# Performance work log

Hardware: AMD Instinct MI355X
Metric: run time of the kernel (lower is better)

## Reference

```python
import jax, jax.numpy as jnp
import numpy as np

RES = 100          # resolution
ITERS = 1000       # lowfid solver iterations
INIT_MIN = 0.01    # conductivity floor (init_min)
BATCH = 32
HIDDEN = [128, 256, 512]


def conductivity_original(pores, res):
    """Coarse 5x5 pore map -> base conductivity on the fine res x res grid.
    pore present (1) -> low conductivity (0), solid (0) -> conductivity 1."""
    B = pores.shape[0]
    grid = 1.0 - pores.reshape(B, 5, 5)
    f = res // 5
    return jnp.repeat(jnp.repeat(grid, f, axis=1), f, axis=2)  # (B, res, res)


def mlp_forward(x, params):
    n = len(params)
    for i, (W, b) in enumerate(params):
        x = x @ W + b
        if i < n - 1:
            x = jax.nn.relu(x)
    return x


def lowfid_solve(k):
    """1000-iteration Jacobi relaxation of variable-coefficient steady heat
    equation with T=1 on top edge, T=0 on bottom edge, insulated sides.
    Returns effective conductivity kappa per sample, shape (B,)."""
    B, res, _ = k.shape
    # face conductivities (arithmetic mean of adjacent cells, edge-padded)
    kp = jnp.pad(k, ((0, 0), (1, 1), (1, 1)), mode='edge')
    kN = 0.5 * (k + kp[:, :-2, 1:-1])
    kS = 0.5 * (k + kp[:, 2:, 1:-1])
    kW = 0.5 * (k + kp[:, 1:-1, :-2])
    kE = 0.5 * (k + kp[:, 1:-1, 2:])
    denom = kN + kS + kW + kE + 1e-12

    def step(T, _):
        Tp = jnp.pad(T, ((0, 0), (0, 0), (1, 1)), mode='edge')        # side Neumann
        Tp = jnp.pad(Tp, ((0, 0), (1, 1), (0, 0)))                    # top/bottom Dirichlet
        Tp = Tp.at[:, 0, :].set(1.0)                                   # T=1 at top, T=0 at bottom
        T_new = (kN * Tp[:, :-2, 1:-1] + kS * Tp[:, 2:, 1:-1]
                 + kW * Tp[:, 1:-1, :-2] + kE * Tp[:, 1:-1, 2:]) / denom
        return T_new, None

    T0 = jnp.broadcast_to(jnp.linspace(1.0, 0.0, res)[None, :, None], (B, res, res))
    T, _ = jax.lax.scan(step, T0, None, length=ITERS)
    # heat flux through top boundary; domain size 1, dT = 1 -> kappa = mean flux
    kappa = jnp.mean(2.0 * res * k[:, 0, :] * (1.0 - T[:, 0, :]), axis=1)
    return kappa


def setup_inputs() -> dict:
    key = jax.random.key(0)
    ks = jax.random.split(key, 10)
    pores = (jax.random.uniform(ks[0], (BATCH, 25)) > 0.5).astype(jnp.float32)
    sizes = [25] + HIDDEN + [RES * RES]
    inp = {"pores": pores}
    for i in range(len(sizes) - 1):
        fan_in = sizes[i]
        W = jax.random.normal(ks[1 + 2 * i], (sizes[i], sizes[i + 1]), jnp.float32) * np.sqrt(2.0 / fan_in)
        b = jnp.zeros((sizes[i + 1],), jnp.float32)
        inp[f"W{i + 1}"] = W
        inp[f"b{i + 1}"] = b
    return inp


def reference(pores, W1, b1, W2, b2, W3, b3, W4, b4):
    params = [(W1, b1), (W2, b2), (W3, b3), (W4, b4)]
    B = pores.shape[0]
    gen = mlp_forward(pores.reshape(B, 25), params).reshape(B, RES, RES)
    cond = gen + conductivity_original(pores, RES)   # learn_residual
    cond = jnp.maximum(cond, INIT_MIN)               # relu clamp to init_min
    kappa = lowfid_solve(cond)
    return kappa, cond
```

## Files before the change

kernel.cpp:

```cpp
#include <hip/hip_runtime.h>
#include <hip/hip_bf16.h>

#define RES   100
#define ITERS 1000
#define SLOTP 128

typedef float vf2 __attribute__((ext_vector_type(2)));

__global__ __launch_bounds__(256) void mlp123(const float* __restrict__ pores,
                                              const float* __restrict__ W1, const float* __restrict__ b1,
                                              const float* __restrict__ W2, const float* __restrict__ b2,
                                              const float* __restrict__ W3, const float* __restrict__ b3,
                                              float* __restrict__ x3out) {
    __shared__ float x1[128];
    __shared__ float x2[256];
    const int s = blockIdx.x, tid = threadIdx.x;

    if (tid < 128) {
        float acc = b1[tid];
#pragma unroll
        for (int k = 0; k < 25; ++k)
            acc = fmaf(pores[s * 25 + k], W1[k * 128 + tid], acc);
        x1[tid] = fmaxf(acc, 0.0f);
    }
    __syncthreads();

    {
        float acc = b2[tid];
#pragma unroll 8
        for (int k = 0; k < 128; ++k)
            acc = fmaf(x1[k], W2[k * 256 + tid], acc);
        x2[tid] = fmaxf(acc, 0.0f);
    }
    __syncthreads();

    {
        float a0 = b3[tid], a1 = b3[tid + 256];
#pragma unroll 8
        for (int k = 0; k < 256; ++k) {
            float xv = x2[k];
            a0 = fmaf(xv, W3[k * 512 + tid],       a0);
            a1 = fmaf(xv, W3[k * 512 + tid + 256], a1);
        }
        x3out[s * 512 + tid]       = fmaxf(a0, 0.0f);
        x3out[s * 512 + tid + 256] = fmaxf(a1, 0.0f);
    }
}

__global__ __launch_bounds__(256) void fc4_fused(const float* __restrict__ X3,
                                                 const float* __restrict__ W4,
                                                 const float* __restrict__ b4,
                                                 const float* __restrict__ pores,
                                                 float* __restrict__ cond) {
    const int j = blockIdx.x * 256 + threadIdx.x;
    if (j >= RES * RES) return;
    const int bg = blockIdx.y;
    const float* x = X3 + bg * 8 * 512;

    float acc[8];
    float bj = b4[j];
#pragma unroll
    for (int b = 0; b < 8; ++b) acc[b] = bj;

    for (int k0 = 0; k0 < 512; k0 += 8) {
        float w[8];
#pragma unroll
        for (int u = 0; u < 8; ++u)
            w[u] = W4[(k0 + u) * (RES * RES) + j];
#pragma unroll
        for (int u = 0; u < 8; ++u) {
#pragma unroll
            for (int b = 0; b < 8; ++b)
                acc[b] = fmaf(x[b * 512 + k0 + u], w[u], acc[b]);
        }
    }

    const int row = j / RES, col = j % RES;
    const int p = (row / 20) * 5 + (col / 20);
#pragma unroll
    for (int b = 0; b < 8; ++b) {
        int bb = bg * 8 + b;
        float base = 1.0f - pores[bb * 25 + p];
        cond[bb * RES * RES + j] = fmaxf(acc[b] + base, 0.01f);
    }
}

__device__ __forceinline__ float dpp_shr1_z(float src) {
    return __int_as_float(__builtin_amdgcn_update_dpp(
        0, __float_as_int(src), 0x138, 0xf, 0xf, true));
}
__device__ __forceinline__ float dpp_shl1_z(float src) {
    return __int_as_float(__builtin_amdgcn_update_dpp(
        0, __float_as_int(src), 0x130, 0xf, 0xf, true));
}

__device__ __forceinline__ vf2 jrowT(vf2 wv, vf2 ev, vf2 c,
                                     vf2 wWr, vf2 wEr, vf2 wPr, vf2 wTr, vf2 Cr) {
    float nlo = dpp_shr1_z(c.y);
    float shi = dpp_shl1_z(c.x);
    vf2 P;  P.x  = nlo; P.y  = shi;
    vf2 TS; TS.x = c.y; TS.y = c.x;
    return Cr + wPr * P + wTr * TS + wWr * wv + wEr * ev;
}

template<int R>
__device__ __forceinline__ void jstepT(const vf2* __restrict__ wptr, const vf2* __restrict__ eptr,
                                       vf2* __restrict__ topptr, vf2* __restrict__ botptr,
                                       const vf2* wW, const vf2* wE,
                                       const vf2* wP, const vf2* wT, const vf2* C,
                                       const vf2* Tin, vf2* Tout) {
    vf2 wval = *wptr;
    vf2 eval = *eptr;
#pragma unroll
    for (int r = 0; r < R; ++r) {
        vf2 wv = (r == 0)     ? wval : Tin[r - 1];
        vf2 ev = (r == R - 1) ? eval : Tin[r + 1];
        Tout[r] = jrowT(wv, ev, Tin[r], wW[r], wE[r], wP[r], wT[r], C[r]);
        if (r == 0) *topptr = Tout[0];
    }
    *botptr = Tout[R - 1];
}

__global__ __launch_bounds__(1024) void jacobi(const float* __restrict__ cond,
                                               float* __restrict__ kappa_out) {
    __shared__ float kst[RES * RES];
    __shared__ float SA[32 * SLOTP];
    __shared__ float SB[32 * SLOTP];
    __shared__ float red[16];

    const int b   = blockIdx.x;
    const int tid = threadIdx.x;

    for (int i = tid; i < RES * RES; i += 1024)
        kst[i] = cond[b * RES * RES + i];
    __syncthreads();

    const int w    = tid >> 6;
    const int lane = tid & 63;
    const int R    = (w < 4) ? 7 : 6;
    const int c0   = (w < 4) ? 7 * w : 28 + 6 * (w - 4);
    const int l    = min(lane, 49);
    const int i0   = 2 * l, i1 = 2 * l + 1;
    const int lane2 = 2 * lane;

    vf2 wW[7], wE[7], wP[7], wT[7], C[7], T0[7], T1[7];

#pragma unroll
    for (int r = 0; r < 7; ++r) {
        if (r < R) {
            int c  = c0 + r;
            int in_ = i0 ? i0 - 1 : 0;
            int is_ = (i1 < RES - 1) ? i1 + 1 : RES - 1;
            int jw  = c ? c - 1 : 0;
            int je  = (c < RES - 1) ? c + 1 : RES - 1;
            float kc0 = kst[i0 * RES + c], kc1 = kst[i1 * RES + c];
            float kn0 = 0.5f * (kc0 + kst[in_ * RES + c]);
            float ks0 = 0.5f * (kc0 + kc1);
            float kw0 = 0.5f * (kc0 + kst[i0 * RES + jw]);
            float ke0 = 0.5f * (kc0 + kst[i0 * RES + je]);
            float kn1 = 0.5f * (kc1 + kc0);
            float ks1 = 0.5f * (kc1 + kst[is_ * RES + c]);
            float kw1 = 0.5f * (kc1 + kst[i1 * RES + jw]);
            float ke1 = 0.5f * (kc1 + kst[i1 * RES + je]);
            float inv0 = 1.0f / (kn0 + ks0 + kw0 + ke0 + 1e-12f);
            float inv1 = 1.0f / (kn1 + ks1 + kw1 + ke1 + 1e-12f);
            wW[r].x = kw0 * inv0;  wW[r].y = kw1 * inv1;
            wE[r].x = ke0 * inv0;  wE[r].y = ke1 * inv1;
            wP[r].x = (l == 0)  ? 0.0f : kn0 * inv0;
            wP[r].y = (l >= 49) ? 0.0f : ks1 * inv1;
            wT[r].x = ks0 * inv0;  wT[r].y = kn1 * inv1;
            C[r].x = (l == 0) ? kn0 * inv0 : 0.0f;
            C[r].y = 0.0f;
            T0[r].x = 1.0f - (float)i0 * (1.0f / (RES - 1));
            T0[r].y = 1.0f - (float)i1 * (1.0f / (RES - 1));
        }
    }

    vf2 bot0 = (w < 4) ? T0[6] : T0[5];
    *(vf2*)(SA + (2 * w) * SLOTP + lane2)     = T0[0];
    *(vf2*)(SA + (2 * w + 1) * SLOTP + lane2) = bot0;
    __syncthreads();

    const int wslot = (w == 0)  ? 0  : (2 * w - 1);
    const int eslot = (w == 15) ? 31 : (2 * w + 2);
    const int topsl = 2 * w;

    const vf2* SAw = (const vf2*)(SA + wslot * SLOTP + lane2);
    const vf2* SAe = (const vf2*)(SA + eslot * SLOTP + lane2);
    const vf2* SBw = (const vf2*)(SB + wslot * SLOTP + lane2);
    const vf2* SBe = (const vf2*)(SB + eslot * SLOTP + lane2);
    vf2* SAtop = (vf2*)(SA + topsl * SLOTP + lane2);
    vf2* SAbot = (vf2*)(SA + (topsl + 1) * SLOTP + lane2);
    vf2* SBtop = (vf2*)(SB + topsl * SLOTP + lane2);
    vf2* SBbot = (vf2*)(SB + (topsl + 1) * SLOTP + lane2);

    for (int it = 0; it < ITERS / 2; ++it) {
        if (w < 4) jstepT<7>(SAw, SAe, SBtop, SBbot, wW, wE, wP, wT, C, T0, T1);
        else       jstepT<6>(SAw, SAe, SBtop, SBbot, wW, wE, wP, wT, C, T0, T1);
        __syncthreads();
        if (w < 4) jstepT<7>(SBw, SBe, SAtop, SAbot, wW, wE, wP, wT, C, T1, T0);
        else       jstepT<6>(SBw, SBe, SAtop, SAbot, wW, wE, wP, wT, C, T1, T0);
        __syncthreads();
    }

    if (lane == 0) {
        float part = 0.0f;
#pragma unroll
        for (int r = 0; r < 7; ++r)
            if (r < R) part = fmaf(kst[c0 + r], 1.0f - T0[r].x, part);
        red[w] = part;
    }
    __syncthreads();
    if (tid == 0) {
        float s = 0.0f;
#pragma unroll
        for (int i = 0; i < 16; ++i) s += red[i];
        kappa_out[b] = 2.0f * s;
    }
}

extern "C" void kernel_launch(void* const* d_in, const int* in_sizes, int n_in,
                              void* d_out, int out_size, void* d_ws, size_t ws_size,
                              hipStream_t stream) {
    (void)in_sizes; (void)n_in; (void)out_size; (void)ws_size;
    const float* pores = (const float*)d_in[0];
    const float* W1 = (const float*)d_in[1];
    const float* b1 = (const float*)d_in[2];
    const float* W2 = (const float*)d_in[3];
    const float* b2 = (const float*)d_in[4];
    const float* W3 = (const float*)d_in[5];
    const float* b3 = (const float*)d_in[6];
    const float* W4 = (const float*)d_in[7];
    const float* b4 = (const float*)d_in[8];

    float* x3 = (float*)d_ws;

    float* kappa = (float*)d_out;
    float* cond  = kappa + 32;

    mlp123<<<32, 256, 0, stream>>>(pores, W1, b1, W2, b2, W3, b3, x3);
    fc4_fused<<<dim3(40, 4), 256, 0, stream>>>(x3, W4, b4, pores, cond);
    jacobi<<<32, 1024, 0, stream>>>(cond, kappa);
}
```

Baseline: 544.8 us.

## Use two-deep halo exchange to halve block barriers in Jacobi loop

Each wavefront now keeps one ghost column on each side, whose coefficients it computes itself. It performs two Jacobi sweeps per shared-memory exchange by swapping two boundary columns at a time. This halves the number of __syncthreads barriers and LDS round trips across the 1000 iterations. In exchange it adds redundant halo computation of about two extra columns per wavefront per round, plus more registers and larger LDS buffers. The edge wavefronts mirror the boundary column to handle the Neumann sides.

```diff
diff --git a/kernel.cpp b/kernel.cpp
--- a/kernel.cpp
+++ b/kernel.cpp
@@ -103,29 +103,48 @@
     return Cr + wPr * P + wTr * TS + wWr * wv + wEr * ev;
 }
 
-template<int R>
-__device__ __forceinline__ void jstepT(const vf2* __restrict__ wptr, const vf2* __restrict__ eptr,
-                                       vf2* __restrict__ topptr, vf2* __restrict__ botptr,
+template<int R, bool HW, bool HE>
+__device__ __forceinline__ void jround(const vf2* __restrict__ wp0, const vf2* __restrict__ wp1,
+                                       const vf2* __restrict__ ep0, const vf2* __restrict__ ep1,
+                                       vf2* __restrict__ ot0, vf2* __restrict__ ot1,
+                                       vf2* __restrict__ ob0, vf2* __restrict__ ob1,
                                        const vf2* wW, const vf2* wE,
                                        const vf2* wP, const vf2* wT, const vf2* C,
-                                       const vf2* Tin, vf2* Tout) {
-    vf2 wval = *wptr;
-    vf2 eval = *eptr;
-#pragma unroll
-    for (int r = 0; r < R; ++r) {
-        vf2 wv = (r == 0)     ? wval : Tin[r - 1];
-        vf2 ev = (r == R - 1) ? eval : Tin[r + 1];
-        Tout[r] = jrowT(wv, ev, Tin[r], wW[r], wE[r], wP[r], wT[r], C[r]);
-        if (r == 0) *topptr = Tout[0];
-    }
-    *botptr = Tout[R - 1];
+                                       vf2* U) {
+    vf2 wv0 = U[1], wv1 = U[1], ev0 = U[R], ev1 = U[R];
+    if constexpr (HW) { wv0 = *wp0; wv1 = *wp1; }
+    if constexpr (HE) { ev0 = *ep0; ev1 = *ep1; }
+
+    vf2 V[R + 2];
+    if constexpr (HW)
+        V[0] = jrowT(wv1, U[1], wv0, wW[0], wE[0], wP[0], wT[0], C[0]);
+#pragma unroll
+    for (int j = 1; j <= R; ++j) {
+        vf2 west = (j == 1) ? (HW ? wv0 : U[1]) : U[j - 1];
+        vf2 east = (j == R) ? (HE ? ev0 : U[R]) : U[j + 1];
+        V[j] = jrowT(west, east, U[j], wW[j], wE[j], wP[j], wT[j], C[j]);
+    }
+    if constexpr (HE)
+        V[R + 1] = jrowT(U[R], ev1, ev0, wW[R + 1], wE[R + 1], wP[R + 1], wT[R + 1], C[R + 1]);
+
+#pragma unroll
+    for (int j = 1; j <= R; ++j) {
+        vf2 west = (j == 1) ? (HW ? V[0] : V[1]) : V[j - 1];
+        vf2 east = (j == R) ? (HE ? V[R + 1] : V[R]) : V[j + 1];
+        U[j] = jrowT(west, east, V[j], wW[j], wE[j], wP[j], wT[j], C[j]);
+    }
+
+    *ot0 = U[1];
+    *ot1 = U[2];
+    *ob1 = U[R - 1];
+    *ob0 = U[R];
 }
 
 __global__ __launch_bounds__(1024) void jacobi(const float* __restrict__ cond,
                                                float* __restrict__ kappa_out) {
     __shared__ float kst[RES * RES];
-    __shared__ float SA[32 * SLOTP];
-    __shared__ float SB[32 * SLOTP];
+    __shared__ float SA[64 * SLOTP];
+    __shared__ float SB[64 * SLOTP];
     __shared__ float red[16];
 
     const int b   = blockIdx.x;
@@ -143,12 +162,13 @@
     const int i0   = 2 * l, i1 = 2 * l + 1;
     const int lane2 = 2 * lane;
 
-    vf2 wW[7], wE[7], wP[7], wT[7], C[7], T0[7], T1[7];
-
-#pragma unroll
-    for (int r = 0; r < 7; ++r) {
-        if (r < R) {
-            int c  = c0 + r;
+    vf2 wW[9], wE[9], wP[9], wT[9], C[9], U[9];
+
+#pragma unroll
+    for (int j = 0; j < 9; ++j) {
+        bool valid = (j >= 1 && j <= R) || (j == 0 && w > 0) || (j == R + 1 && w < 15);
+        if (j <= R + 1 && valid) {
+            int c   = c0 - 1 + j;
             int in_ = i0 ? i0 - 1 : 0;
             int is_ = (i1 < RES - 1) ? i1 + 1 : RES - 1;
             int jw  = c ? c - 1 : 0;
@@ -164,42 +184,55 @@
             float ke1 = 0.5f * (kc1 + kst[i1 * RES + je]);
             float inv0 = 1.0f / (kn0 + ks0 + kw0 + ke0 + 1e-12f);
             float inv1 = 1.0f / (kn1 + ks1 + kw1 + ke1 + 1e-12f);
-            wW[r].x = kw0 * inv0;  wW[r].y = kw1 * inv1;
-            wE[r].x = ke0 * inv0;  wE[r].y = ke1 * inv1;
-            wP[r].x = (l == 0)  ? 0.0f : kn0 * inv0;
-            wP[r].y = (l >= 49) ? 0.0f : ks1 * inv1;
-            wT[r].x = ks0 * inv0;  wT[r].y = kn1 * inv1;
-            C[r].x = (l == 0) ? kn0 * inv0 : 0.0f;
-            C[r].y = 0.0f;
-            T0[r].x = 1.0f - (float)i0 * (1.0f / (RES - 1));
-            T0[r].y = 1.0f - (float)i1 * (1.0f / (RES - 1));
+            wW[j].x = kw0 * inv0;  wW[j].y = kw1 * inv1;
+            wE[j].x = ke0 * inv0;  wE[j].y = ke1 * inv1;
+            wP[j].x = (l == 0)  ? 0.0f : kn0 * inv0;
+            wP[j].y = (l >= 49) ? 0.0f : ks1 * inv1;
+            wT[j].x = ks0 * inv0;  wT[j].y = kn1 * inv1;
+            C[j].x  = (l == 0) ? kn0 * inv0 : 0.0f;
+            C[j].y  = 0.0f;
         }
     }
-
-    vf2 bot0 = (w < 4) ? T0[6] : T0[5];
-    *(vf2*)(SA + (2 * w) * SLOTP + lane2)     = T0[0];
-    *(vf2*)(SA + (2 * w + 1) * SLOTP + lane2) = bot0;
-    __syncthreads();
-
-    const int wslot = (w == 0)  ? 0  : (2 * w - 1);
-    const int eslot = (w == 15) ? 31 : (2 * w + 2);
-    const int topsl = 2 * w;
-
-    const vf2* SAw = (const vf2*)(SA + wslot * SLOTP + lane2);
-    const vf2* SAe = (const vf2*)(SA + eslot * SLOTP + lane2);
-    const vf2* SBw = (const vf2*)(SB + wslot * SLOTP + lane2);
-    const vf2* SBe = (const vf2*)(SB + eslot * SLOTP + lane2);
-    vf2* SAtop = (vf2*)(SA + topsl * SLOTP + lane2);
-    vf2* SAbot = (vf2*)(SA + (topsl + 1) * SLOTP + lane2);
-    vf2* SBtop = (vf2*)(SB + topsl * SLOTP + lane2);
-    vf2* SBbot = (vf2*)(SB + (topsl + 1) * SLOTP + lane2);
-
-    for (int it = 0; it < ITERS / 2; ++it) {
-        if (w < 4) jstepT<7>(SAw, SAe, SBtop, SBbot, wW, wE, wP, wT, C, T0, T1);
-        else       jstepT<6>(SAw, SAe, SBtop, SBbot, wW, wE, wP, wT, C, T0, T1);
+    {
+        float vx = 1.0f - (float)i0 * (1.0f / (RES - 1));
+        float vy = 1.0f - (float)i1 * (1.0f / (RES - 1));
+#pragma unroll
+        for (int j = 0; j < 9; ++j) { U[j].x = vx; U[j].y = vy; }
+    }
+
+    const int wm = (w > 0)  ? w - 1 : 0;
+    const int wpn = (w < 15) ? w + 1 : 15;
+    const vf2* Aw0 = (const vf2*)(SA + (4 * wm + 2) * SLOTP + lane2);
+    const vf2* Aw1 = (const vf2*)(SA + (4 * wm + 3) * SLOTP + lane2);
+    const vf2* Ae0 = (const vf2*)(SA + (4 * wpn + 0) * SLOTP + lane2);
+    const vf2* Ae1 = (const vf2*)(SA + (4 * wpn + 1) * SLOTP + lane2);
+    const vf2* Bw0 = (const vf2*)(SB + (4 * wm + 2) * SLOTP + lane2);
+    const vf2* Bw1 = (const vf2*)(SB + (4 * wm + 3) * SLOTP + lane2);
+    const vf2* Be0 = (const vf2*)(SB + (4 * wpn + 0) * SLOTP + lane2);
+    const vf2* Be1 = (const vf2*)(SB + (4 * wpn + 1) * SLOTP + lane2);
+    vf2* At0 = (vf2*)(SA + (4 * w + 0) * SLOTP + lane2);
+    vf2* At1 = (vf2*)(SA + (4 * w + 1) * SLOTP + lane2);
+    vf2* Ab0 = (vf2*)(SA + (4 * w + 2) * SLOTP + lane2);
+    vf2* Ab1 = (vf2*)(SA + (4 * w + 3) * SLOTP + lane2);
+    vf2* Bt0 = (vf2*)(SB + (4 * w + 0) * SLOTP + lane2);
+    vf2* Bt1 = (vf2*)(SB + (4 * w + 1) * SLOTP + lane2);
+    vf2* Bb0 = (vf2*)(SB + (4 * w + 2) * SLOTP + lane2);
+    vf2* Bb1 = (vf2*)(SB + (4 * w + 3) * SLOTP + lane2);
+
+    *At0 = U[1];  *At1 = U[2];
+    *Ab1 = U[R - 1];  *Ab0 = U[R];
+    __syncthreads();
+
+    for (int it = 0; it < ITERS / 4; ++it) {
+        if      (w == 0)  jround<7, false, true >(Aw0, Aw1, Ae0, Ae1, Bt0, Bt1, Bb0, Bb1, wW, wE, wP, wT, C, U);
+        else if (w < 4)   jround<7, true , true >(Aw0, Aw1, Ae0, Ae1, Bt0, Bt1, Bb0, Bb1, wW, wE, wP, wT, C, U);
+        else if (w < 15)  jround<6, true , true >(Aw0, Aw1, Ae0, Ae1, Bt0, Bt1, Bb0, Bb1, wW, wE, wP, wT, C, U);
+        else              jround<6, true , false>(Aw0, Aw1, Ae0, Ae1, Bt0, Bt1, Bb0, Bb1, wW, wE, wP, wT, C, U);
         __syncthreads();
-        if (w < 4) jstepT<7>(SBw, SBe, SAtop, SAbot, wW, wE, wP, wT, C, T1, T0);
-        else       jstepT<6>(SBw, SBe, SAtop, SAbot, wW, wE, wP, wT, C, T1, T0);
+        if      (w == 0)  jround<7, false, true >(Bw0, Bw1, Be0, Be1, At0, At1, Ab0, Ab1, wW, wE, wP, wT, C, U);
+        else if (w < 4)   jround<7, true , true >(Bw0, Bw1, Be0, Be1, At0, At1, Ab0, Ab1, wW, wE, wP, wT, C, U);
+        else if (w < 15)  jround<6, true , true >(Bw0, Bw1, Be0, Be1, At0, At1, Ab0, Ab1, wW, wE, wP, wT, C, U);
+        else              jround<6, true , false>(Bw0, Bw1, Be0, Be1, At0, At1, Ab0, Ab1, wW, wE, wP, wT, C, U);
         __syncthreads();
     }
 
@@ -207,7 +240,7 @@
         float part = 0.0f;
 #pragma unroll
         for (int r = 0; r < 7; ++r)
-            if (r < R) part = fmaf(kst[c0 + r], 1.0f - T0[r].x, part);
+            if (r < R) part = fmaf(kst[c0 + r], 1.0f - U[r + 1].x, part);
         red[w] = part;
     }
     __syncthreads();
```

Measured after the change: 562.8 us. 1.03x slower.
